# Performance work log

Measured on AMD Instinct MI355X. Metric: run time of the kernel, lower is better.

## Reference

```python
import jax, jax.numpy as jnp
import numpy as np

# Module constants (from source defaults)
RING = 256      # ring_len
D = 128         # slot_dim
IN = 64         # input_dim
SD = max(8, D // 3)  # sensory_dim = 42
K = 2           # gauss_k -> 2K+1 = 5 taps
TAU = 8.0       # gauss_tau
NC = 1000       # num_classes
B, T = 512, 512


def setup_inputs() -> dict:
    key = jax.random.key(0)
    ks = jax.random.split(key, 10)
    g = lambda k, shape, s=0.05: jax.random.normal(k, shape, jnp.float32) * s
    return {
        "x": jax.random.normal(ks[0], (B, T, IN), jnp.float32),
        "theta_ptr": jnp.array([37.0], jnp.float32),
        "w_proj": g(ks[1], (SD, IN)), "b_proj": jnp.zeros((SD,), jnp.float32),
        "w_ih": g(ks[2], (3 * SD, SD)), "w_hh": g(ks[3], (3 * SD, SD)),
        "b_ih": jnp.zeros((3 * SD,), jnp.float32), "b_hh": jnp.zeros((3 * SD,), jnp.float32),
        "w_bridge": g(ks[4], (D, SD)), "b_bridge": jnp.zeros((D,), jnp.float32),
        "w_jump": g(ks[5], (1, D)), "b_jump": jnp.zeros((1,), jnp.float32),
        "w_gate": g(ks[6], (1, D)), "b_gate": jnp.zeros((1,), jnp.float32),
        "w_cls": g(ks[7], (NC, D)), "b_cls": jnp.zeros((NC,), jnp.float32),
    }


def _kernel(ptr):
    """Gaussian soft window around a fractional ring pointer. ptr: [B] float."""
    offs = jnp.arange(-K, K + 1)
    base = jnp.floor(ptr)
    frac = ptr - base                               # [B]
    pos = jnp.mod(base.astype(jnp.int32)[:, None] + offs[None, :], RING)  # [B, 2K+1]
    d = offs.astype(ptr.dtype)[None, :] - frac[:, None]
    w = jax.nn.softmax(-(d * d) / TAU, axis=-1)     # [B, 2K+1]
    return pos, w


def reference(x, theta_ptr, w_proj, b_proj, w_ih, w_hh, b_ih, b_hh,
              w_bridge, b_bridge, w_jump, b_jump, w_gate, b_gate, w_cls, b_cls):
    Bn = x.shape[0]
    bidx = jnp.arange(Bn)
    ring0 = jnp.zeros((Bn, RING, D), x.dtype)
    h0 = jnp.zeros((Bn, SD), x.dtype)
    ptr0 = jnp.broadcast_to(jnp.mod(theta_ptr, float(RING)), (Bn,)).astype(x.dtype)

    def step(carry, xt):
        ring, h, ptr = carry
        # sensory path: Linear -> GRUCell -> bridge
        s = xt @ w_proj.T + b_proj
        gx = s @ w_ih.T + b_ih
        gh = h @ w_hh.T + b_hh
        rg = jax.nn.sigmoid(gx[:, :SD] + gh[:, :SD])
        zg = jax.nn.sigmoid(gx[:, SD:2 * SD] + gh[:, SD:2 * SD])
        ng = jnp.tanh(gx[:, 2 * SD:] + rg * gh[:, 2 * SD:])
        h = (1.0 - zg) * ng + zg * h
        u = jnp.tanh(h @ w_bridge.T + b_bridge)      # write vector [B, D]
        # soft-kernel read at current pointer
        pos, w = _kernel(ptr)
        r = jnp.einsum('bk,bkd->bd', w, ring[bidx[:, None], pos])
        # pointer jump target + gate, circ_lerp along shortest arc
        jump = jax.nn.sigmoid(r @ w_jump.T + b_jump)[:, 0] * RING
        gate = jax.nn.sigmoid(r @ w_gate.T + b_gate)[:, 0]
        delta = jnp.mod(jump - ptr + RING / 2.0, float(RING)) - RING / 2.0  # wrap_delta
        ptr = jnp.mod(ptr + gate * delta, float(RING))                      # circ_lerp
        # soft-kernel write at new pointer
        pos2, w2 = _kernel(ptr)
        ring = ring.at[bidx[:, None], pos2].add(w2[..., None] * u[:, None, :])
        return (ring, h, ptr), None

    (ring, h, ptr), _ = jax.lax.scan(step, (ring0, h0, ptr0), jnp.swapaxes(x, 0, 1))
    pos, w = _kernel(ptr)
    r = jnp.einsum('bk,bkd->bd', w, ring[bidx[:, None], pos])
    return r @ w_cls.T + b_cls
```

## Files before the change

kernel.cpp:

```cpp
#include <hip/hip_runtime.h>
#include <hip/hip_bf16.h>
#include <cstdint>

#define RINGN 256
#define DD    128
#define SDN   42
#define G3N   126
#define INN   64
#define BN    512
#define TN    512
#define NCN   1000
#define HS    44
#define GXS   128
#define BT    (BN * TN)

typedef float v2f __attribute__((ext_vector_type(2)));
typedef float4 __attribute__((may_alias)) f4ma;
typedef float2 __attribute__((may_alias)) f2ma;

__device__ __forceinline__ float sigm(float x)    { return 1.0f / (1.0f + __expf(-x)); }
__device__ __forceinline__ float tanhfast(float x){ float e = __expf(2.0f * x); return 1.0f - 2.0f / (e + 1.0f); }
__device__ __forceinline__ float wrap256(float x) { return x - 256.0f * floorf(x * 0.00390625f); }

__device__ __forceinline__ void taps_norm(float p, int* pos, float* w) {
  float base = floorf(p);
  float frac = p - base;
  int ib = (int)base;
  float e[5];
  float s = 0.0f;
#pragma unroll
  for (int k = 0; k < 5; k++) {
    float d = (float)(k - 2) - frac;
    e[k] = __expf(-(d * d) * 0.125f);
    s += e[k];
    pos[k] = (ib + k - 2) & 255;
  }
  float inv = 1.0f / s;
#pragma unroll
  for (int k = 0; k < 5; k++) w[k] = e[k] * inv;
}

template<int C>
__device__ __forceinline__ float dpp_add_step(float x) {
  int t = __builtin_amdgcn_update_dpp(0, __float_as_int(x), C, 0xf, 0xf, true);
  return x + __int_as_float(t);
}
__device__ __forceinline__ float wave_sum64(float x) {
  x = dpp_add_step<0x111>(x);
  x = dpp_add_step<0x112>(x);
  x = dpp_add_step<0x114>(x);
  x = dpp_add_step<0x118>(x);
  x = dpp_add_step<0x142>(x);
  x = dpp_add_step<0x143>(x);
  return __int_as_float(__builtin_amdgcn_readlane(__float_as_int(x), 63));
}

__global__ void prep_kernel(const float* __restrict__ w_ih, const float* __restrict__ w_proj,
                            const float* __restrict__ b_proj, const float* __restrict__ b_ih,
                            float* __restrict__ Wc, float* __restrict__ bc) {
  int idx = blockIdx.x * 256 + threadIdx.x;
  if (idx < G3N * INN) {
    int j = idx / INN, i = idx % INN;
    float a = 0.0f;
    for (int k = 0; k < SDN; k++) a += w_ih[j * SDN + k] * w_proj[k * INN + i];
    Wc[idx] = a;
  }
  if (idx < G3N) {
    float a = b_ih[idx];
    for (int k = 0; k < SDN; k++) a += w_ih[idx * SDN + k] * b_proj[k];
    bc[idx] = a;
  }
}

__global__ __launch_bounds__(256)
void gx_gemm(const float* __restrict__ x, const float* __restrict__ Wc,
             const float* __restrict__ bc, float* __restrict__ gxp) {
  __shared__ __align__(16) float WcS[G3N * INN];
  __shared__ float bcS[G3N + 2];
  __shared__ float tileS[256 * 33];
  const int tid = threadIdx.x;
  const float4* wc4 = (const float4*)Wc;
  float4* wcs4 = (float4*)WcS;
  for (int i = tid; i < G3N * INN / 4; i += 256) wcs4[i] = wc4[i];
  if (tid < G3N) bcS[tid] = bc[tid];
  __syncthreads();

  const size_t row0 = (size_t)blockIdx.x * 256;
  const size_t row = row0 + tid;
  v2f xr[INN / 2];
#pragma unroll
  for (int i = 0; i < INN / 4; i++) {
    float4 v = *reinterpret_cast<const float4*>(&x[row * INN + i * 4]);
    xr[2 * i]     = (v2f){v.x, v.y};
    xr[2 * i + 1] = (v2f){v.z, v.w};
  }

  for (int c0 = 0; c0 < GXS; c0 += 32) {
#pragma unroll
    for (int cc = 0; cc < 32; cc++) {
      int c = c0 + cc;
      float val = 0.0f;
      if (c < G3N) {
        const v2f* w = (const v2f*)&WcS[c * INN];
        v2f acc2 = (v2f){bcS[c], 0.0f};
#pragma unroll
        for (int i = 0; i < INN / 2; i++) acc2 = __builtin_elementwise_fma(w[i], xr[i], acc2);
        val = acc2.x + acc2.y;
      }
      tileS[tid * 33 + cc] = val;
    }
    __syncthreads();
#pragma unroll
    for (int i = 0; i < 8; i++) {
      int f = i * 256 + tid;
      int r = f >> 3;
      int cc4 = (f & 7) * 4;
      float4 v = make_float4(tileS[r * 33 + cc4], tileS[r * 33 + cc4 + 1],
                             tileS[r * 33 + cc4 + 2], tileS[r * 33 + cc4 + 3]);
      *reinterpret_cast<float4*>(&gxp[(row0 + r) * GXS + c0 + cc4]) = v;
    }
    __syncthreads();
  }
}

__global__ __launch_bounds__(128, 1)
void rec2_kernel(const float* __restrict__ gxp,
                 const float* __restrict__ w_hh, const float* __restrict__ b_hh,
                 const float* __restrict__ w_bridge, const float* __restrict__ b_bridge,
                 const float* __restrict__ w_jump, const float* __restrict__ b_jump,
                 const float* __restrict__ w_gate, const float* __restrict__ b_gate,
                 const float* __restrict__ theta,
                 float* __restrict__ hbuf, float* __restrict__ ptrbuf) {
  const int tid = threadIdx.x;
  const int wid = tid >> 6;
  const int lane = tid & 63;
  const int b = blockIdx.x;

  __shared__ float2 JG[RINGN];
  __shared__ __align__(16) float h_buf[HS];
  __shared__ float ringJ[TN];
  __shared__ float ringG[TN];
  __shared__ int ready;

  if (wid == 0) {
    if (lane < HS) h_buf[lane] = 0.0f;
    if (lane == 0) ready = 0;
  } else {
    for (int i = lane; i < RINGN; i += 64) JG[i] = make_float2(0.f, 0.f);
  }
  __syncthreads();

  if (wid == 0) {
    const int jj = (lane < SDN) ? lane : (SDN - 1);
    const int r1 = lane + 64;

    const v2f* whh2 = (const v2f*)w_hh;
    const v2f* wb2  = (const v2f*)w_bridge;
    v2f Whr[21], Whz[21], Whn[21], Wb0[21], Wb1[21];
#pragma unroll
    for (int k = 0; k < 21; k++) {
      Whr[k] = whh2[jj * 21 + k];
      Whz[k] = whh2[(jj + SDN) * 21 + k];
      Whn[k] = whh2[(jj + 2 * SDN) * 21 + k];
      Wb0[k] = wb2[lane * 21 + k];
      Wb1[k] = wb2[r1 * 21 + k];
    }
    const float bhr = b_hh[jj], bhz = b_hh[jj + SDN], bhn = b_hh[jj + 2 * SDN];
    const float bb0 = b_bridge[lane], bb1 = b_bridge[r1];
    const float wj0 = w_jump[lane], wj1 = w_jump[r1];
    const float wg0 = w_gate[lane], wg1 = w_gate[r1];

    v2f hv2[22];
#pragma unroll
    for (int k = 0; k < 22; k++) hv2[k] = (v2f){0.f, 0.f};
    float hprev = 0.0f;

    const float* gxr = gxp + (size_t)b * TN * GXS;
    const int o0 = jj, o1 = SDN + jj, o2 = 2 * SDN + jj;
    float* hb = hbuf + (size_t)b * TN * HS;

    float pA0 = gxr[o0], pA1 = gxr[o1], pA2 = gxr[o2];
    float pB0 = gxr[GXS + o0], pB1 = gxr[GXS + o1], pB2 = gxr[GXS + o2];

    volatile float* rj = ringJ;
    volatile float* rg = ringG;
    volatile int* rdy = &ready;

    auto STEP = [&](int t, float pgx0, float pgx1, float pgx2) {
      v2f ar = (v2f){bhr, 0.f}, az = (v2f){bhz, 0.f}, an = (v2f){bhn, 0.f};
#pragma unroll
      for (int k = 0; k < 21; k++) {
        v2f h2 = hv2[k];
        ar = __builtin_elementwise_fma(Whr[k], h2, ar);
        az = __builtin_elementwise_fma(Whz[k], h2, az);
        an = __builtin_elementwise_fma(Whn[k], h2, an);
      }
      float ghr = ar.x + ar.y, ghz = az.x + az.y, ghn = an.x + an.y;
      float rgate = sigm(pgx0 + ghr);
      float zg = sigm(pgx1 + ghz);
      float ng = tanhfast(pgx2 + rgate * ghn);
      float hn = (1.0f - zg) * ng + zg * hprev;
      hprev = hn;
      if (lane < SDN) {
        h_buf[lane] = hn;
        hb[(size_t)t * HS + lane] = hn;
      }
      __builtin_amdgcn_wave_barrier();
      asm volatile("" ::: "memory");

#pragma unroll
      for (int i = 0; i < 11; i++) {
        float4 v = *(const f4ma*)(&h_buf[i * 4]);
        hv2[2 * i]     = (v2f){v.x, v.y};
        hv2[2 * i + 1] = (v2f){v.z, v.w};
      }

      v2f a0 = (v2f){bb0, 0.f}, a1 = (v2f){bb1, 0.f};
#pragma unroll
      for (int k = 0; k < 21; k++) {
        v2f h2 = hv2[k];
        a0 = __builtin_elementwise_fma(Wb0[k], h2, a0);
        a1 = __builtin_elementwise_fma(Wb1[k], h2, a1);
      }
      float u0 = tanhfast(a0.x + a0.y);
      float u1 = tanhfast(a1.x + a1.y);

      float pjs = wave_sum64(u0 * wj0 + u1 * wj1);
      float pgs = wave_sum64(u0 * wg0 + u1 * wg1);

      if (lane == 0) { rj[t] = pjs; rg[t] = pgs; }
      asm volatile("s_waitcnt lgkmcnt(0)" ::: "memory");
      if (lane == 0) *rdy = t + 1;
    };

    for (int t = 0; t < TN; t += 2) {
      STEP(t, pA0, pA1, pA2);
      if (t + 2 < TN) {
        const float* g = gxr + (size_t)(t + 2) * GXS;
        pA0 = g[o0]; pA1 = g[o1]; pA2 = g[o2];
      }
      STEP(t + 1, pB0, pB1, pB2);
      if (t + 3 < TN) {
        const float* g = gxr + (size_t)(t + 3) * GXS;
        pB0 = g[o0]; pB1 = g[o1]; pB2 = g[o2];
      }
    }
  } else {
    const float bj = b_jump[0], bg = b_gate[0];
    float ptr = wrap256(theta[0]);
    float* pb = ptrbuf + (size_t)b * TN;

    float wk[5]; float2 Vk[5];
    {
      int posk[5];
      taps_norm(ptr, posk, wk);
#pragma unroll
      for (int k = 0; k < 5; k++) Vk[k] = JG[posk[k]];
    }
    float pjprev = 0.f, pgprev = 0.f, S2prev = 0.f;
    volatile int* rdy = &ready;
    int seen = 0;

    for (int t = 0; t < TN; t++) {
      float dotJ = 0.f, dotG = 0.f;
#pragma unroll
      for (int k = 0; k < 5; k++) { dotJ += wk[k] * Vk[k].x; dotG += wk[k] * Vk[k].y; }
      float Jv = fmaf(pjprev, S2prev, dotJ);
      float Gv = fmaf(pgprev, S2prev, dotG);
      float jump = 256.0f * sigm(Jv + bj);
      float gate = sigm(Gv + bg);
      float delta = wrap256(jump - ptr + 128.0f) - 128.0f;
      float ptr2 = wrap256(ptr + gate * delta);

      float tbase = floorf(ptr2);
      float frac = ptr2 - tbase;
      int ib = (int)tbase;
      float e2[5], ssum = 0.f; int pos2[5];
#pragma unroll
      for (int k = 0; k < 5; k++) {
        float d = (float)(k - 2) - frac;
        e2[k] = __expf(-(d * d) * 0.125f);
        ssum += e2[k];
        pos2[k] = (ib + k - 2) & 255;
      }
      float inv2 = 1.0f / ssum;
      float2 Vk2[5];
#pragma unroll
      for (int k = 0; k < 5; k++) Vk2[k] = JG[pos2[k]];
      float w2n[5], S2 = 0.f;
#pragma unroll
      for (int k = 0; k < 5; k++) { w2n[k] = e2[k] * inv2; S2 = fmaf(w2n[k], w2n[k], S2); }
      if (lane == 0) pb[t] = ptr2;

      if (seen <= t) {
        while ((seen = *rdy) <= t) __builtin_amdgcn_s_sleep(1);
      }
      asm volatile("" ::: "memory");
      float pjs = ringJ[t];
      float pgs = ringG[t];

      int p2sel = pos2[0]; float w2sel = w2n[0];
#pragma unroll
      for (int k = 1; k < 5; k++) {
        if (lane == k) { p2sel = pos2[k]; w2sel = w2n[k]; }
      }
      if (lane < 5) {
        atomicAdd(&JG[p2sel].x, w2sel * pjs);
        atomicAdd(&JG[p2sel].y, w2sel * pgs);
      }

#pragma unroll
      for (int k = 0; k < 5; k++) { wk[k] = w2n[k]; Vk[k] = Vk2[k]; }
      S2prev = S2; pjprev = pjs; pgprev = pgs; ptr = ptr2;
    }
  }
}

__global__ __launch_bounds__(64)
void rfinal_kernel(const float* __restrict__ hbuf, const float* __restrict__ ptrbuf,
                   const float* __restrict__ w_bridge, const float* __restrict__ b_bridge,
                   float* __restrict__ rbuf) {
  const int b = blockIdx.x;
  const int chunk = blockIdx.y;
  const int lane = threadIdx.x;
  const int t0 = chunk * 128;
  const int r1 = lane + 64;

  __shared__ float c_lds[128];

  const float* pb = ptrbuf + (size_t)b * TN;
  float ptrf = pb[TN - 1];
  int posf[5]; float wf[5];
  taps_norm(ptrf, posf, wf);

#pragma unroll
  for (int rr = 0; rr < 2; rr++) {
    int tt = rr * 64 + lane;
    int p2[5]; float w2[5];
    taps_norm(pb[t0 + tt], p2, w2);
    float c = 0.0f;
#pragma unroll
    for (int k = 0; k < 5; k++)
#pragma unroll
      for (int k2 = 0; k2 < 5; k2++)
        c += (posf[k] == p2[k2]) ? wf[k] * w2[k2] : 0.0f;
    c_lds[tt] = c;
  }
  __builtin_amdgcn_wave_barrier();
  asm volatile("" ::: "memory");

  const v2f* wb2 = (const v2f*)w_bridge;
  v2f Wb0[21], Wb1[21];
#pragma unroll
  for (int k = 0; k < 21; k++) { Wb0[k] = wb2[lane * 21 + k]; Wb1[k] = wb2[r1 * 21 + k]; }
  float bb0 = b_bridge[lane], bb1 = b_bridge[r1];

  float racc0 = 0.0f, racc1 = 0.0f;
  for (int tt = 0; tt < 128; tt++) {
    float ct = c_lds[tt];
    if (ct != 0.0f) {
      const f4ma* hp = (const f4ma*)(hbuf + ((size_t)b * TN + t0 + tt) * HS);
      v2f hx[22];
#pragma unroll
      for (int i = 0; i < 11; i++) {
        float4 v = hp[i];
        hx[2 * i]     = (v2f){v.x, v.y};
        hx[2 * i + 1] = (v2f){v.z, v.w};
      }
      v2f a0 = (v2f){bb0, 0.f}, a1 = (v2f){bb1, 0.f};
#pragma unroll
      for (int k = 0; k < 21; k++) {
        a0 = __builtin_elementwise_fma(Wb0[k], hx[k], a0);
        a1 = __builtin_elementwise_fma(Wb1[k], hx[k], a1);
      }
      racc0 += ct * tanhfast(a0.x + a0.y);
      racc1 += ct * tanhfast(a1.x + a1.y);
    }
  }
  atomicAdd(&rbuf[b * DD + lane], racc0);
  atomicAdd(&rbuf[b * DD + 64 + lane], racc1);
}

__global__ __launch_bounds__(256)
void cls_kernel(const float* __restrict__ rbuf, const float* __restrict__ w_cls,
                const float* __restrict__ b_cls, float* __restrict__ out) {
  const int b0 = blockIdx.x * 4;
  const int tid = threadIdx.x;
  __shared__ __align__(16) float r[4 * DD];
  for (int i = tid; i < 4 * DD; i += 256) r[i] = rbuf[(size_t)b0 * DD + i];
  __syncthreads();

  for (int c = tid; c < NCN; c += 256) {
    float bcv = b_cls[c];
    float a0 = bcv, a1 = bcv, a2 = bcv, a3 = bcv;
    const float* wrow = &w_cls[(size_t)c * DD];
#pragma unroll
    for (int d4 = 0; d4 < DD / 4; d4++) {
      float4 wv = *reinterpret_cast<const float4*>(&wrow[d4 * 4]);
      float4 r0 = *(const f4ma*)(&r[0 * DD + d4 * 4]);
      float4 r1 = *(const f4ma*)(&r[1 * DD + d4 * 4]);
      float4 r2 = *(const f4ma*)(&r[2 * DD + d4 * 4]);
      float4 r3 = *(const f4ma*)(&r[3 * DD + d4 * 4]);
      a0 += wv.x * r0.x + wv.y * r0.y + wv.z * r0.z + wv.w * r0.w;
      a1 += wv.x * r1.x + wv.y * r1.y + wv.z * r1.z + wv.w * r1.w;
      a2 += wv.x * r2.x + wv.y * r2.y + wv.z * r2.z + wv.w * r2.w;
      a3 += wv.x * r3.x + wv.y * r3.y + wv.z * r3.z + wv.w * r3.w;
    }
    out[(size_t)(b0 + 0) * NCN + c] = a0;
    out[(size_t)(b0 + 1) * NCN + c] = a1;
    out[(size_t)(b0 + 2) * NCN + c] = a2;
    out[(size_t)(b0 + 3) * NCN + c] = a3;
  }
}

extern "C" void kernel_launch(void* const* d_in, const int* in_sizes, int n_in,
                              void* d_out, int out_size, void* d_ws, size_t ws_size,
                              hipStream_t stream) {
  const float* x        = (const float*)d_in[0];
  const float* theta    = (const float*)d_in[1];
  const float* w_proj   = (const float*)d_in[2];
  const float* b_proj   = (const float*)d_in[3];
  const float* w_ih     = (const float*)d_in[4];
  const float* w_hh     = (const float*)d_in[5];
  const float* b_ih     = (const float*)d_in[6];
  const float* b_hh     = (const float*)d_in[7];
  const float* w_bridge = (const float*)d_in[8];
  const float* b_bridge = (const float*)d_in[9];
  const float* w_jump   = (const float*)d_in[10];
  const float* b_jump   = (const float*)d_in[11];
  const float* w_gate   = (const float*)d_in[12];
  const float* b_gate   = (const float*)d_in[13];
  const float* w_cls    = (const float*)d_in[14];
  const float* b_cls    = (const float*)d_in[15];
  float* out = (float*)d_out;

  char* ws = (char*)d_ws;
  size_t off = 0;
  float* gxp    = (float*)(ws + off); off += (size_t)BT * GXS * 4;
  float* hbuf   = (float*)(ws + off); off += (size_t)BN * TN * HS * 4;
  float* ptrbuf = (float*)(ws + off); off += (size_t)BN * TN * 4;
  float* rbuf   = (float*)(ws + off); off += (size_t)BN * DD * 4;
  float* Wc     = (float*)(ws + off); off += (((size_t)G3N * INN * 4 + 255) & ~(size_t)255);
  float* bc     = (float*)(ws + off); off += 512;

  hipMemsetAsync(rbuf, 0, (size_t)BN * DD * 4, stream);
  prep_kernel<<<32, 256, 0, stream>>>(w_ih, w_proj, b_proj, b_ih, Wc, bc);
  gx_gemm<<<BT / 256, 256, 0, stream>>>(x, Wc, bc, gxp);
  rec2_kernel<<<BN, 128, 0, stream>>>(gxp, w_hh, b_hh, w_bridge, b_bridge,
                                      w_jump, b_jump, w_gate, b_gate, theta, hbuf, ptrbuf);
  dim3 gfin(BN, 4);
  rfinal_kernel<<<gfin, 64, 0, stream>>>(hbuf, ptrbuf, w_bridge, b_bridge, rbuf);
  cls_kernel<<<BN / 4, 256, 0, stream>>>(rbuf, w_cls, b_cls, out);
}
```

Measured before the change: 622.9 us.

## Split GRU and bridge projection into separate pipelined wavefronts

The recurrent kernel grows from two to three wavefronts. Wave 0 now runs only the GRU recurrence and writes each hidden state into a 32-slot shared ring. A new wave 1 consumes those states to compute the bridge, tanh and jump/gate reductions, and wave 2 still runs the pointer recurrence. This takes the bridge matvec and wave reductions off the GRU's critical path, at the cost of flag-based spin synchronisation, a backpressure check and one more wave per block.

```diff
diff --git a/kernel.cpp b/kernel.cpp
--- a/kernel.cpp
+++ b/kernel.cpp
@@ -13,6 +13,7 @@
 #define HS    44
 #define GXS   128
 #define BT    (BN * TN)
+#define HSLOTS 32
 
 typedef float v2f __attribute__((ext_vector_type(2)));
 typedef float4 __attribute__((may_alias)) f4ma;
@@ -123,8 +124,8 @@
   }
 }
 
-__global__ __launch_bounds__(128, 1)
-void rec2_kernel(const float* __restrict__ gxp,
+__global__ __launch_bounds__(192, 1)
+void rec3_kernel(const float* __restrict__ gxp,
                  const float* __restrict__ w_hh, const float* __restrict__ b_hh,
                  const float* __restrict__ w_bridge, const float* __restrict__ b_bridge,
                  const float* __restrict__ w_jump, const float* __restrict__ b_jump,
@@ -137,38 +138,27 @@
   const int b = blockIdx.x;
 
   __shared__ float2 JG[RINGN];
-  __shared__ __align__(16) float h_buf[HS];
+  __shared__ __align__(16) float h_ring[HSLOTS * HS];
   __shared__ float ringJ[TN];
   __shared__ float ringG[TN];
-  __shared__ int ready;
-
-  if (wid == 0) {
-    if (lane < HS) h_buf[lane] = 0.0f;
-    if (lane == 0) ready = 0;
-  } else {
-    for (int i = lane; i < RINGN; i += 64) JG[i] = make_float2(0.f, 0.f);
-  }
+  __shared__ int flagH;
+  __shared__ int done1;
+
+  if (tid == 0) { flagH = 0; done1 = 0; }
   __syncthreads();
 
   if (wid == 0) {
     const int jj = (lane < SDN) ? lane : (SDN - 1);
-    const int r1 = lane + 64;
 
     const v2f* whh2 = (const v2f*)w_hh;
-    const v2f* wb2  = (const v2f*)w_bridge;
-    v2f Whr[21], Whz[21], Whn[21], Wb0[21], Wb1[21];
+    v2f Whr[21], Whz[21], Whn[21];
 #pragma unroll
     for (int k = 0; k < 21; k++) {
       Whr[k] = whh2[jj * 21 + k];
       Whz[k] = whh2[(jj + SDN) * 21 + k];
       Whn[k] = whh2[(jj + 2 * SDN) * 21 + k];
-      Wb0[k] = wb2[lane * 21 + k];
-      Wb1[k] = wb2[r1 * 21 + k];
     }
     const float bhr = b_hh[jj], bhz = b_hh[jj + SDN], bhn = b_hh[jj + 2 * SDN];
-    const float bb0 = b_bridge[lane], bb1 = b_bridge[r1];
-    const float wj0 = w_jump[lane], wj1 = w_jump[r1];
-    const float wg0 = w_gate[lane], wg1 = w_gate[r1];
 
     v2f hv2[22];
 #pragma unroll
@@ -182,11 +172,13 @@
     float pA0 = gxr[o0], pA1 = gxr[o1], pA2 = gxr[o2];
     float pB0 = gxr[GXS + o0], pB1 = gxr[GXS + o1], pB2 = gxr[GXS + o2];
 
-    volatile float* rj = ringJ;
-    volatile float* rg = ringG;
-    volatile int* rdy = &ready;
+    volatile int* fH = &flagH;
+    volatile int* fC = &done1;
 
     auto STEP = [&](int t, float pgx0, float pgx1, float pgx2) {
+      if ((t & 7) == 0 && t >= HSLOTS) {
+        while (*fC < t - 24) __builtin_amdgcn_s_sleep(1);
+      }
       v2f ar = (v2f){bhr, 0.f}, az = (v2f){bhz, 0.f}, an = (v2f){bhn, 0.f};
 #pragma unroll
       for (int k = 0; k < 21; k++) {
@@ -201,36 +193,23 @@
       float ng = tanhfast(pgx2 + rgate * ghn);
       float hn = (1.0f - zg) * ng + zg * hprev;
       hprev = hn;
+
+      float* slot = &h_ring[(t & (HSLOTS - 1)) * HS];
       if (lane < SDN) {
-        h_buf[lane] = hn;
+        slot[lane] = hn;
         hb[(size_t)t * HS + lane] = hn;
       }
+      asm volatile("s_waitcnt lgkmcnt(0)" ::: "memory");
+      if (lane == 0) *fH = t + 1;
       __builtin_amdgcn_wave_barrier();
       asm volatile("" ::: "memory");
 
 #pragma unroll
       for (int i = 0; i < 11; i++) {
-        float4 v = *(const f4ma*)(&h_buf[i * 4]);
+        float4 v = *(const f4ma*)(&slot[i * 4]);
         hv2[2 * i]     = (v2f){v.x, v.y};
         hv2[2 * i + 1] = (v2f){v.z, v.w};
       }
-
-      v2f a0 = (v2f){bb0, 0.f}, a1 = (v2f){bb1, 0.f};
-#pragma unroll
-      for (int k = 0; k < 21; k++) {
-        v2f h2 = hv2[k];
-        a0 = __builtin_elementwise_fma(Wb0[k], h2, a0);
-        a1 = __builtin_elementwise_fma(Wb1[k], h2, a1);
-      }
-      float u0 = tanhfast(a0.x + a0.y);
-      float u1 = tanhfast(a1.x + a1.y);
-
-      float pjs = wave_sum64(u0 * wj0 + u1 * wj1);
-      float pgs = wave_sum64(u0 * wg0 + u1 * wg1);
-
-      if (lane == 0) { rj[t] = pjs; rg[t] = pgs; }
-      asm volatile("s_waitcnt lgkmcnt(0)" ::: "memory");
-      if (lane == 0) *rdy = t + 1;
     };
 
     for (int t = 0; t < TN; t += 2) {
@@ -245,7 +224,58 @@
         pB0 = g[o0]; pB1 = g[o1]; pB2 = g[o2];
       }
     }
+  } else if (wid == 1) {
+    const int r1 = lane + 64;
+    const v2f* wb2 = (const v2f*)w_bridge;
+    v2f Wb0[21], Wb1[21];
+#pragma unroll
+    for (int k = 0; k < 21; k++) {
+      Wb0[k] = wb2[lane * 21 + k];
+      Wb1[k] = wb2[r1 * 21 + k];
+    }
+    const float bb0 = b_bridge[lane], bb1 = b_bridge[r1];
+    const float wj0 = w_jump[lane], wj1 = w_jump[r1];
+    const float wg0 = w_gate[lane], wg1 = w_gate[r1];
+
+    volatile int* fH = &flagH;
+    volatile int* fC = &done1;
+    int seenH = 0;
+
+    for (int t = 0; t < TN; t++) {
+      if (seenH <= t) {
+        while ((seenH = *fH) <= t) __builtin_amdgcn_s_sleep(1);
+      }
+      asm volatile("" ::: "memory");
+      const float* slot = &h_ring[(t & (HSLOTS - 1)) * HS];
+      v2f hw[22];
+#pragma unroll
+      for (int i = 0; i < 11; i++) {
+        float4 v = *(const f4ma*)(&slot[i * 4]);
+        hw[2 * i]     = (v2f){v.x, v.y};
+        hw[2 * i + 1] = (v2f){v.z, v.w};
+      }
+      v2f a0 = (v2f){bb0, 0.f}, a1 = (v2f){bb1, 0.f};
+#pragma unroll
+      for (int k = 0; k < 21; k++) {
+        v2f h2 = hw[k];
+        a0 = __builtin_elementwise_fma(Wb0[k], h2, a0);
+        a1 = __builtin_elementwise_fma(Wb1[k], h2, a1);
+      }
+      float u0 = tanhfast(a0.x + a0.y);
+      float u1 = tanhfast(a1.x + a1.y);
+
+      float pjs = wave_sum64(u0 * wj0 + u1 * wj1);
+      float pgs = wave_sum64(u0 * wg0 + u1 * wg1);
+
+      if (lane == 0) { ringJ[t] = pjs; ringG[t] = pgs; }
+      asm volatile("s_waitcnt lgkmcnt(0)" ::: "memory");
+      if (lane == 0) *fC = t + 1;
+    }
   } else {
+    for (int i = lane; i < RINGN; i += 64) JG[i] = make_float2(0.f, 0.f);
+    __builtin_amdgcn_wave_barrier();
+    asm volatile("" ::: "memory");
+
     const float bj = b_jump[0], bg = b_gate[0];
     float ptr = wrap256(theta[0]);
     float* pb = ptrbuf + (size_t)b * TN;
@@ -258,7 +288,7 @@
       for (int k = 0; k < 5; k++) Vk[k] = JG[posk[k]];
     }
     float pjprev = 0.f, pgprev = 0.f, S2prev = 0.f;
-    volatile int* rdy = &ready;
+    volatile int* rdy = &done1;
     int seen = 0;
 
     for (int t = 0; t < TN; t++) {
@@ -446,9 +476,9 @@
   hipMemsetAsync(rbuf, 0, (size_t)BN * DD * 4, stream);
   prep_kernel<<<32, 256, 0, stream>>>(w_ih, w_proj, b_proj, b_ih, Wc, bc);
   gx_gemm<<<BT / 256, 256, 0, stream>>>(x, Wc, bc, gxp);
-  rec2_kernel<<<BN, 128, 0, stream>>>(gxp, w_hh, b_hh, w_bridge, b_bridge,
+  rec3_kernel<<<BN, 192, 0, stream>>>(gxp, w_hh, b_hh, w_bridge, b_bridge,
                                       w_jump, b_jump, w_gate, b_gate, theta, hbuf, ptrbuf);
   dim3 gfin(BN, 4);
-  rfinal_kernel<<<gfin, 64, 0, stream>>>(hbuf, ptrbuf, w_bridge, b_bridge, rbuf);
+  rfinal_kernel<<<gfin, 4 * 16, 0, stream>>>(hbuf, ptrbuf, w_bridge, b_bridge, rbuf);
   cls_kernel<<<BN / 4, 256, 0, stream>>>(rbuf, w_cls, b_cls, out);
 }
```

Result: faster. 543.4 us (-12.8%).

## Split recurrence into three-wave software pipeline with per-step block barrier

Applied to the files above, without the earlier changes.

The recurrent kernel goes from two waves to three: the GRU, the bridge/jump-gate projection and the pointer update each run on their own wave, staggered by one step and joined by a workgroup barrier each iteration. Small ring buffers in shared memory pass hidden states and jump/gate scalars between stages, replacing the spin-wait flag. The aim is to shorten the serial critical path by moving the bridge matvec off the GRU wave and overlapping the three stages. In exchange every step now pays a full s_barrier, and the slowest stage sets the pace.

```diff
diff --git a/kernel.cpp b/kernel.cpp
--- a/kernel.cpp
+++ b/kernel.cpp
@@ -123,8 +123,8 @@
   }
 }
 
-__global__ __launch_bounds__(128, 1)
-void rec2_kernel(const float* __restrict__ gxp,
+__global__ __launch_bounds__(192, 1)
+void rec3_kernel(const float* __restrict__ gxp,
                  const float* __restrict__ w_hh, const float* __restrict__ b_hh,
                  const float* __restrict__ w_bridge, const float* __restrict__ b_bridge,
                  const float* __restrict__ w_jump, const float* __restrict__ b_jump,
@@ -137,182 +137,179 @@
   const int b = blockIdx.x;
 
   __shared__ float2 JG[RINGN];
-  __shared__ __align__(16) float h_buf[HS];
-  __shared__ float ringJ[TN];
-  __shared__ float ringG[TN];
-  __shared__ int ready;
-
-  if (wid == 0) {
-    if (lane < HS) h_buf[lane] = 0.0f;
-    if (lane == 0) ready = 0;
-  } else {
-    for (int i = lane; i < RINGN; i += 64) JG[i] = make_float2(0.f, 0.f);
-  }
-  __syncthreads();
+  __shared__ __align__(16) float h_ring[4 * HS];
+  __shared__ float2 pjring[4];
+
+  v2f Whr[21], Whz[21], Whn[21];
+  float bhr = 0.f, bhz = 0.f, bhn = 0.f;
+  v2f hv2[22];
+  float hprev = 0.0f;
+  const float* gxr = gxp + (size_t)b * TN * GXS;
+  float* hb = hbuf + (size_t)b * TN * HS;
+  int o0 = 0, o1 = 0, o2 = 0;
+  float cu0 = 0.f, cu1 = 0.f, cu2 = 0.f, n10 = 0.f, n11 = 0.f, n12 = 0.f;
+  v2f Wb0[21], Wb1[21];
+  float bb0 = 0.f, bb1 = 0.f, wj0 = 0.f, wj1 = 0.f, wg0 = 0.f, wg1 = 0.f;
+  float bj = 0.f, bg = 0.f, ptr = 0.f;
+  float* pb = ptrbuf + (size_t)b * TN;
+  float wk[5]; float2 Vk[5];
+  float pjprev = 0.f, pgprev = 0.f, S2prev = 0.f;
 
   if (wid == 0) {
     const int jj = (lane < SDN) ? lane : (SDN - 1);
-    const int r1 = lane + 64;
-
     const v2f* whh2 = (const v2f*)w_hh;
-    const v2f* wb2  = (const v2f*)w_bridge;
-    v2f Whr[21], Whz[21], Whn[21], Wb0[21], Wb1[21];
 #pragma unroll
     for (int k = 0; k < 21; k++) {
       Whr[k] = whh2[jj * 21 + k];
       Whz[k] = whh2[(jj + SDN) * 21 + k];
       Whn[k] = whh2[(jj + 2 * SDN) * 21 + k];
+    }
+    bhr = b_hh[jj]; bhz = b_hh[jj + SDN]; bhn = b_hh[jj + 2 * SDN];
+#pragma unroll
+    for (int k = 0; k < 22; k++) hv2[k] = (v2f){0.f, 0.f};
+    o0 = jj; o1 = SDN + jj; o2 = 2 * SDN + jj;
+    cu0 = gxr[o0]; cu1 = gxr[o1]; cu2 = gxr[o2];
+    n10 = gxr[GXS + o0]; n11 = gxr[GXS + o1]; n12 = gxr[GXS + o2];
+  } else if (wid == 1) {
+    const int r1 = lane + 64;
+    const v2f* wb2 = (const v2f*)w_bridge;
+#pragma unroll
+    for (int k = 0; k < 21; k++) {
       Wb0[k] = wb2[lane * 21 + k];
       Wb1[k] = wb2[r1 * 21 + k];
     }
-    const float bhr = b_hh[jj], bhz = b_hh[jj + SDN], bhn = b_hh[jj + 2 * SDN];
-    const float bb0 = b_bridge[lane], bb1 = b_bridge[r1];
-    const float wj0 = w_jump[lane], wj1 = w_jump[r1];
-    const float wg0 = w_gate[lane], wg1 = w_gate[r1];
-
-    v2f hv2[22];
-#pragma unroll
-    for (int k = 0; k < 22; k++) hv2[k] = (v2f){0.f, 0.f};
-    float hprev = 0.0f;
-
-    const float* gxr = gxp + (size_t)b * TN * GXS;
-    const int o0 = jj, o1 = SDN + jj, o2 = 2 * SDN + jj;
-    float* hb = hbuf + (size_t)b * TN * HS;
-
-    float pA0 = gxr[o0], pA1 = gxr[o1], pA2 = gxr[o2];
-    float pB0 = gxr[GXS + o0], pB1 = gxr[GXS + o1], pB2 = gxr[GXS + o2];
-
-    volatile float* rj = ringJ;
-    volatile float* rg = ringG;
-    volatile int* rdy = &ready;
-
-    auto STEP = [&](int t, float pgx0, float pgx1, float pgx2) {
-      v2f ar = (v2f){bhr, 0.f}, az = (v2f){bhz, 0.f}, an = (v2f){bhn, 0.f};
-#pragma unroll
-      for (int k = 0; k < 21; k++) {
-        v2f h2 = hv2[k];
-        ar = __builtin_elementwise_fma(Whr[k], h2, ar);
-        az = __builtin_elementwise_fma(Whz[k], h2, az);
-        an = __builtin_elementwise_fma(Whn[k], h2, an);
-      }
-      float ghr = ar.x + ar.y, ghz = az.x + az.y, ghn = an.x + an.y;
-      float rgate = sigm(pgx0 + ghr);
-      float zg = sigm(pgx1 + ghz);
-      float ng = tanhfast(pgx2 + rgate * ghn);
-      float hn = (1.0f - zg) * ng + zg * hprev;
-      hprev = hn;
-      if (lane < SDN) {
-        h_buf[lane] = hn;
-        hb[(size_t)t * HS + lane] = hn;
-      }
-      __builtin_amdgcn_wave_barrier();
-      asm volatile("" ::: "memory");
-
-#pragma unroll
-      for (int i = 0; i < 11; i++) {
-        float4 v = *(const f4ma*)(&h_buf[i * 4]);
-        hv2[2 * i]     = (v2f){v.x, v.y};
-        hv2[2 * i + 1] = (v2f){v.z, v.w};
-      }
-
-      v2f a0 = (v2f){bb0, 0.f}, a1 = (v2f){bb1, 0.f};
-#pragma unroll
-      for (int k = 0; k < 21; k++) {
-        v2f h2 = hv2[k];
-        a0 = __builtin_elementwise_fma(Wb0[k], h2, a0);
-        a1 = __builtin_elementwise_fma(Wb1[k], h2, a1);
-      }
-      float u0 = tanhfast(a0.x + a0.y);
-      float u1 = tanhfast(a1.x + a1.y);
-
-      float pjs = wave_sum64(u0 * wj0 + u1 * wj1);
-      float pgs = wave_sum64(u0 * wg0 + u1 * wg1);
-
-      if (lane == 0) { rj[t] = pjs; rg[t] = pgs; }
-      asm volatile("s_waitcnt lgkmcnt(0)" ::: "memory");
-      if (lane == 0) *rdy = t + 1;
-    };
-
-    for (int t = 0; t < TN; t += 2) {
-      STEP(t, pA0, pA1, pA2);
-      if (t + 2 < TN) {
-        const float* g = gxr + (size_t)(t + 2) * GXS;
-        pA0 = g[o0]; pA1 = g[o1]; pA2 = g[o2];
-      }
-      STEP(t + 1, pB0, pB1, pB2);
-      if (t + 3 < TN) {
-        const float* g = gxr + (size_t)(t + 3) * GXS;
-        pB0 = g[o0]; pB1 = g[o1]; pB2 = g[o2];
-      }
-    }
+    bb0 = b_bridge[lane]; bb1 = b_bridge[r1];
+    wj0 = w_jump[lane]; wj1 = w_jump[r1];
+    wg0 = w_gate[lane]; wg1 = w_gate[r1];
   } else {
-    const float bj = b_jump[0], bg = b_gate[0];
-    float ptr = wrap256(theta[0]);
-    float* pb = ptrbuf + (size_t)b * TN;
-
-    float wk[5]; float2 Vk[5];
+    for (int i = lane; i < RINGN; i += 64) JG[i] = make_float2(0.f, 0.f);
+    bj = b_jump[0]; bg = b_gate[0];
+    ptr = wrap256(theta[0]);
     {
       int posk[5];
       taps_norm(ptr, posk, wk);
 #pragma unroll
       for (int k = 0; k < 5; k++) Vk[k] = JG[posk[k]];
     }
-    float pjprev = 0.f, pgprev = 0.f, S2prev = 0.f;
-    volatile int* rdy = &ready;
-    int seen = 0;
-
-    for (int t = 0; t < TN; t++) {
-      float dotJ = 0.f, dotG = 0.f;
-#pragma unroll
-      for (int k = 0; k < 5; k++) { dotJ += wk[k] * Vk[k].x; dotG += wk[k] * Vk[k].y; }
-      float Jv = fmaf(pjprev, S2prev, dotJ);
-      float Gv = fmaf(pgprev, S2prev, dotG);
-      float jump = 256.0f * sigm(Jv + bj);
-      float gate = sigm(Gv + bg);
-      float delta = wrap256(jump - ptr + 128.0f) - 128.0f;
-      float ptr2 = wrap256(ptr + gate * delta);
-
-      float tbase = floorf(ptr2);
-      float frac = ptr2 - tbase;
-      int ib = (int)tbase;
-      float e2[5], ssum = 0.f; int pos2[5];
-#pragma unroll
-      for (int k = 0; k < 5; k++) {
-        float d = (float)(k - 2) - frac;
-        e2[k] = __expf(-(d * d) * 0.125f);
-        ssum += e2[k];
-        pos2[k] = (ib + k - 2) & 255;
-      }
-      float inv2 = 1.0f / ssum;
-      float2 Vk2[5];
-#pragma unroll
-      for (int k = 0; k < 5; k++) Vk2[k] = JG[pos2[k]];
-      float w2n[5], S2 = 0.f;
-#pragma unroll
-      for (int k = 0; k < 5; k++) { w2n[k] = e2[k] * inv2; S2 = fmaf(w2n[k], w2n[k], S2); }
-      if (lane == 0) pb[t] = ptr2;
-
-      if (seen <= t) {
-        while ((seen = *rdy) <= t) __builtin_amdgcn_s_sleep(1);
-      }
-      asm volatile("" ::: "memory");
-      float pjs = ringJ[t];
-      float pgs = ringG[t];
-
-      int p2sel = pos2[0]; float w2sel = w2n[0];
-#pragma unroll
-      for (int k = 1; k < 5; k++) {
-        if (lane == k) { p2sel = pos2[k]; w2sel = w2n[k]; }
-      }
-      if (lane < 5) {
-        atomicAdd(&JG[p2sel].x, w2sel * pjs);
-        atomicAdd(&JG[p2sel].y, w2sel * pgs);
-      }
-
-#pragma unroll
-      for (int k = 0; k < 5; k++) { wk[k] = w2n[k]; Vk[k] = Vk2[k]; }
-      S2prev = S2; pjprev = pjs; pgprev = pgs; ptr = ptr2;
-    }
+  }
+
+  for (int i = 0; i <= TN + 1; i++) {
+    if (wid == 0) {
+      if (i < TN) {
+        const int t = i;
+        v2f ar = (v2f){bhr, 0.f}, az = (v2f){bhz, 0.f}, an = (v2f){bhn, 0.f};
+#pragma unroll
+        for (int k = 0; k < 21; k++) {
+          v2f h2 = hv2[k];
+          ar = __builtin_elementwise_fma(Whr[k], h2, ar);
+          az = __builtin_elementwise_fma(Whz[k], h2, az);
+          an = __builtin_elementwise_fma(Whn[k], h2, an);
+        }
+        float ghr = ar.x + ar.y, ghz = az.x + az.y, ghn = an.x + an.y;
+        float rgate = sigm(cu0 + ghr);
+        float zg = sigm(cu1 + ghz);
+        float ng = tanhfast(cu2 + rgate * ghn);
+        float hn = (1.0f - zg) * ng + zg * hprev;
+        hprev = hn;
+
+        float* slot = &h_ring[(t & 3) * HS];
+        if (lane < SDN) {
+          slot[lane] = hn;
+          hb[(size_t)t * HS + lane] = hn;
+        }
+        __builtin_amdgcn_wave_barrier();
+        asm volatile("" ::: "memory");
+#pragma unroll
+        for (int k4 = 0; k4 < 11; k4++) {
+          float4 v = *(const f4ma*)(&slot[k4 * 4]);
+          hv2[2 * k4]     = (v2f){v.x, v.y};
+          hv2[2 * k4 + 1] = (v2f){v.z, v.w};
+        }
+        cu0 = n10; cu1 = n11; cu2 = n12;
+        if (t + 2 < TN) {
+          const float* g = gxr + (size_t)(t + 2) * GXS;
+          n10 = g[o0]; n11 = g[o1]; n12 = g[o2];
+        }
+      }
+    } else if (wid == 1) {
+      if (i >= 1 && i <= TN) {
+        const int t = i - 1;
+        const float* slot = &h_ring[(t & 3) * HS];
+        v2f hw[22];
+#pragma unroll
+        for (int k4 = 0; k4 < 11; k4++) {
+          float4 v = *(const f4ma*)(&slot[k4 * 4]);
+          hw[2 * k4]     = (v2f){v.x, v.y};
+          hw[2 * k4 + 1] = (v2f){v.z, v.w};
+        }
+        v2f a0 = (v2f){bb0, 0.f}, a1 = (v2f){bb1, 0.f};
+#pragma unroll
+        for (int k = 0; k < 21; k++) {
+          v2f h2 = hw[k];
+          a0 = __builtin_elementwise_fma(Wb0[k], h2, a0);
+          a1 = __builtin_elementwise_fma(Wb1[k], h2, a1);
+        }
+        float u0 = tanhfast(a0.x + a0.y);
+        float u1 = tanhfast(a1.x + a1.y);
+        float pjs = wave_sum64(u0 * wj0 + u1 * wj1);
+        float pgs = wave_sum64(u0 * wg0 + u1 * wg1);
+        if (lane == 0) pjring[t & 3] = make_float2(pjs, pgs);
+      }
+    } else {
+      if (i >= 2) {
+        const int t = i - 2;
+        float dotJ = 0.f, dotG = 0.f;
+#pragma unroll
+        for (int k = 0; k < 5; k++) { dotJ += wk[k] * Vk[k].x; dotG += wk[k] * Vk[k].y; }
+        float Jv = fmaf(pjprev, S2prev, dotJ);
+        float Gv = fmaf(pgprev, S2prev, dotG);
+        float jump = 256.0f * sigm(Jv + bj);
+        float gate = sigm(Gv + bg);
+        float delta = wrap256(jump - ptr + 128.0f) - 128.0f;
+        float ptr2 = wrap256(ptr + gate * delta);
+
+        float tbase = floorf(ptr2);
+        float frac = ptr2 - tbase;
+        int ib = (int)tbase;
+        float e2[5], ssum = 0.f; int pos2[5];
+#pragma unroll
+        for (int k = 0; k < 5; k++) {
+          float d = (float)(k - 2) - frac;
+          e2[k] = __expf(-(d * d) * 0.125f);
+          ssum += e2[k];
+          pos2[k] = (ib + k - 2) & 255;
+        }
+        float inv2 = 1.0f / ssum;
+        float2 Vk2[5];
+#pragma unroll
+        for (int k = 0; k < 5; k++) Vk2[k] = JG[pos2[k]];
+        float w2n[5], S2 = 0.f;
+#pragma unroll
+        for (int k = 0; k < 5; k++) { w2n[k] = e2[k] * inv2; S2 = fmaf(w2n[k], w2n[k], S2); }
+        if (lane == 0) pb[t] = ptr2;
+
+        float2 pp = pjring[t & 3];
+        float pjs = pp.x, pgs = pp.y;
+
+        int p2sel = pos2[0]; float w2sel = w2n[0];
+#pragma unroll
+        for (int k = 1; k < 5; k++) {
+          if (lane == k) { p2sel = pos2[k]; w2sel = w2n[k]; }
+        }
+        if (lane < 5) {
+          atomicAdd(&JG[p2sel].x, w2sel * pjs);
+          atomicAdd(&JG[p2sel].y, w2sel * pgs);
+        }
+
+#pragma unroll
+        for (int k = 0; k < 5; k++) { wk[k] = w2n[k]; Vk[k] = Vk2[k]; }
+        S2prev = S2; pjprev = pjs; pgprev = pgs; ptr = ptr2;
+      }
+    }
+
+    asm volatile("s_waitcnt lgkmcnt(0)" ::: "memory");
+    __builtin_amdgcn_s_barrier();
+    asm volatile("" ::: "memory");
   }
 }
 
@@ -446,7 +443,7 @@
   hipMemsetAsync(rbuf, 0, (size_t)BN * DD * 4, stream);
   prep_kernel<<<32, 256, 0, stream>>>(w_ih, w_proj, b_proj, b_ih, Wc, bc);
   gx_gemm<<<BT / 256, 256, 0, stream>>>(x, Wc, bc, gxp);
-  rec2_kernel<<<BN, 128, 0, stream>>>(gxp, w_hh, b_hh, w_bridge, b_bridge,
+  rec3_kernel<<<BN, 192, 0, stream>>>(gxp, w_hh, b_hh, w_bridge, b_bridge,
                                       w_jump, b_jump, w_gate, b_gate, theta, hbuf, ptrbuf);
   dim3 gfin(BN, 4);
   rfinal_kernel<<<gfin, 64, 0, stream>>>(hbuf, ptrbuf, w_bridge, b_bridge, rbuf);
```

Result: slower. 899.2 us (+44.4%).
